# Kernel tuning notes

Hardware: AMD Instinct MI355X
Metric: run time of the kernel (lower is better)

The kernel has to match this reference:

```python
import jax, jax.numpy as jnp
import numpy as np

K = 3  # kernel size along all four dims (kernel_size=3, padding=2=K-1, circular)


def setup_inputs() -> dict:
    key = jax.random.key(0)
    k1, k2, k3 = jax.random.split(key, 3)
    b, c_in, c_out, s = 4, 64, 64, 16
    x = jax.random.normal(k1, (b, c_in, s, s, s, s), dtype=jnp.float32)
    # torch grouped Conv3d weight (out_c*K, c_in, K, K, K) viewed as (K, out_c, c_in, K, K, K):
    # group g (= kernel slice along dim 0) uses weight[g].
    weight = jax.random.normal(k2, (K, c_out, c_in, K, K, K), dtype=jnp.float32) * 0.05
    bias = jax.random.normal(k3, (c_out,), dtype=jnp.float32)
    return {"x": x, "weight": weight, "bias": bias}


def _conv4d_circular(x, weight, bias):
    k = weight.shape[0]
    p = k - 1
    lo, hi = (p + 1) // 2, p // 2  # circular pad split used by do_padding
    b, c = x.shape[0], x.shape[1]
    s0, s1, s2, s3 = x.shape[2:]
    c_out = weight.shape[1]
    # circular-pad the three inner spatial dims only (dim s0 handled via rolls)
    xp = jnp.pad(x, ((0, 0), (0, 0), (0, 0), (lo, hi), (lo, hi), (lo, hi)), mode='wrap')
    # fold s0 into batch: (b*s0, c, S1, S2, S3)
    xr = xp.transpose(0, 2, 1, 3, 4, 5).reshape(b * s0, c, s1 + p, s2 + p, s3 + p)
    # grouped conv with input replicated across groups == k independent VALID 3D convs
    conv = lambda w: jax.lax.conv_general_dilated(
        xr, w, window_strides=(1, 1, 1), padding='VALID',
        dimension_numbers=('NCDHW', 'OIDHW', 'NCDHW'))
    out = jax.vmap(conv)(weight)  # (k, b*s0, c_out, s1, s2, s3)
    out = out.reshape(k, b, s0, c_out, s1, s2, s3).transpose(0, 1, 3, 2, 4, 5, 6)
    # combine kernel slices along dim-0 axis: result[..., t] = sum_i out[i, ..., (t+i) % s0]
    rolled = jnp.stack([jnp.roll(out[i], -i, axis=2) for i in range(k)], axis=0)
    res = rolled.sum(axis=0) + bias[None, :, None, None, None, None]
    shift = (p + 1) // 2  # math.ceil(padding[0] / 2)
    res = jnp.roll(res, shift, axis=2)
    return res  # (b, c_out, s0, s1, s2, s3)


def reference(x, weight, bias):
    return _conv4d_circular(x, weight, bias)
```

## Files before the change

### kernel.cpp

```cpp
#include <hip/hip_runtime.h>

typedef unsigned short u16;
typedef __attribute__((ext_vector_type(8))) __bf16 bf16x8;
typedef __attribute__((ext_vector_type(8))) short short8;
typedef __attribute__((ext_vector_type(4))) short short4v;
typedef __attribute__((ext_vector_type(4))) float floatx4;

__device__ __forceinline__ u16 f2bf(float f){
  unsigned int x = __float_as_uint(f);
  unsigned int r = (x + 0x7fffu + ((x >> 16) & 1u)) >> 16;
  return (u16)r;
}

#define GLL(g, l) __builtin_amdgcn_global_load_lds( \
    (const __attribute__((address_space(1))) void*)(g), \
    (__attribute__((address_space(3))) void*)(l), 16, 0, 0)

__global__ void prep_kernel(const float* __restrict__ x, const float* __restrict__ w,
                            u16* __restrict__ xp, u16* __restrict__ wp){
  __shared__ __attribute__((aligned(16))) u16 I[16384];
  const int bx = blockIdx.x;
  const int tid = threadIdx.x;
  if (bx < 1024){
    const int y = bx & 15, t = (bx >> 4) & 15, b = bx >> 8;
    const int l  = tid & 63;
    const int wv = tid >> 6;
    const float* xb = x + (size_t)b*64*65536 + t*4096 + y*256;

#pragma unroll
    for (int j = 0; j < 16; ++j){
      const int ci = j*4 + wv;
      const float4 f = *(const float4*)(xb + (size_t)ci*65536 + l*4);
      const int o  = ci >> 3;
      const int gp = l ^ o ^ ((o & 1) << 3);
      short4v hv;
      hv[0] = (short)f2bf(f.x);
      hv[1] = (short)f2bf(f.y);
      hv[2] = (short)f2bf(f.z);
      hv[3] = (short)f2bf(f.w);
      *(short4v*)(I + ci*256 + gp*4) = hv;
    }
    __syncthreads();

    const int p  = tid & 7;
    const int r0 = tid >> 3;
    u16* dst = xp + (size_t)bx*16384;
#pragma unroll
    for (int it = 0; it < 8; ++it){
      const int zw = it*32 + r0;
      const int o  = p ^ (zw & 7);
      const int g  = zw >> 2;
      const int gp = g ^ o ^ ((o & 1) << 3);
      const int base = gp*4 + (zw & 3);
      short8 vv;
#pragma unroll
      for (int m = 0; m < 8; ++m)
        vv[m] = (short)I[(o*8 + m)*256 + base];
      *(short8*)(dst + it*2048 + tid*8) = vv;
    }
  } else {
    int idx = (bx - 1024)*256 + tid;
    if (idx < 81*64*64){
      int r  = idx;
      int dw = r % 3; r /= 3;
      int dz = r % 3; r /= 3;
      int dy = r % 3; r /= 3;
      int ci = r & 63; r >>= 6;
      int co = r & 63; r >>= 6;
      int dt = r;
      int tap = ((dt*3 + dy)*3 + dz)*3 + dw;
      int kc = ci >> 5, ci32 = ci & 31;
      wp[tap*4096 + kc*2048 + co*32 + ci32] = f2bf(w[idx]);
    }
  }
}

__global__ __launch_bounds__(256, 2) void conv4d_mfma_v4(
    const u16* __restrict__ xp, const u16* __restrict__ wp,
    const float* __restrict__ bias, float* __restrict__ out)
{
  __shared__ __attribute__((aligned(16))) u16 x_lds[16384];
  __shared__ __attribute__((aligned(16))) u16 a_lds[2][12288];

  const int bx = blockIdx.x;
  const int c = bx & 7, j = bx >> 3;
  const int b = c >> 1, t = j >> 3, y = (c & 1)*8 + (j & 7);

  const int tid  = threadIdx.x;
  const int lane = tid & 63;
  const int wv   = tid >> 6;
  const int wl   = lane & 15;
  const int q    = lane >> 4;

  floatx4 acc[4][4];
#pragma unroll
  for (int zi = 0; zi < 4; ++zi)
#pragma unroll
    for (int mi = 0; mi < 4; ++mi)
      acc[zi][mi] = (floatx4)0.0f;

  auto stage_x = [&](int dtdy){
    const int dt = dtdy / 3, dy = dtdy % 3;
    const int tt = (t + dt + 15) & 15;
    const int yy = (y + dy + 15) & 15;
    const u16* plane = xp + (size_t)(((b*16 + tt)*16) + yy) * 16384;
#pragma unroll
    for (int i = 0; i < 8; ++i)
      GLL(plane + wv*4096 + i*512 + lane*8, x_lds + wv*4096 + i*512);
  };
  auto stage_a = [&](int s, int buf){
    const int dtdy = s / 3, dz = s % 3;
    const int tap0 = ((dtdy/3)*9 + (dtdy%3)*3 + dz)*3;
    const u16* asrc = wp + (size_t)tap0 * 4096;
#pragma unroll
    for (int i = 0; i < 6; ++i)
      GLL(asrc + wv*3072 + i*512 + lane*8, a_lds[buf] + wv*3072 + i*512);
  };

  stage_x(0);
  stage_a(0, 0);
  __syncthreads();

  for (int s = 0; s < 27; ++s){
    const int dz  = s % 3;
    const int cur = s & 1;
    const bool boundary = (dz == 2);
    if (s + 1 < 27 && !boundary)
      stage_a(s + 1, cur ^ 1);

    const u16* ab = a_lds[cur];
#pragma unroll
    for (int dw = 0; dw < 3; ++dw){
      const int ww = (wl + dw + 15) & 15;
      const int wx = ww & 7;
#pragma unroll
      for (int kc = 0; kc < 2; ++kc){
        bf16x8 af[4];
#pragma unroll
        for (int mi = 0; mi < 4; ++mi)
          af[mi] = *(const bf16x8*)(ab + ((dw*2 + kc)*64 + mi*16 + wl)*32 + q*8);
        const int chunk = ((kc*4 + q) ^ wx)*8;
#pragma unroll
        for (int zi = 0; zi < 4; ++zi){
          const int zz = (wv*4 + zi + dz + 15) & 15;
          bf16x8 bf = *(const bf16x8*)(x_lds + (zz*16 + ww)*64 + chunk);
#pragma unroll
          for (int mi = 0; mi < 4; ++mi)
            acc[zi][mi] = __builtin_amdgcn_mfma_f32_16x16x32_bf16(af[mi], bf, acc[zi][mi], 0, 0, 0);
        }
      }
    }

    if (s + 1 >= 27) break;
    if (boundary){
      __syncthreads();
      stage_x(s/3 + 1);
      stage_a(s + 1, cur ^ 1);
      __syncthreads();
    } else {
      __syncthreads();
    }
  }

  float bvals[4][4];
#pragma unroll
  for (int mi = 0; mi < 4; ++mi)
#pragma unroll
    for (int r = 0; r < 4; ++r)
      bvals[mi][r] = bias[mi*16 + q*4 + r];

  float* ob = out + (size_t)b*64*65536 + t*4096 + y*256 + wl;
#pragma unroll
  for (int zi = 0; zi < 4; ++zi){
    const int z = wv*4 + zi;
#pragma unroll
    for (int mi = 0; mi < 4; ++mi){
#pragma unroll
      for (int r = 0; r < 4; ++r){
        const int co = mi*16 + q*4 + r;
        ob[(size_t)co*65536 + z*16] = acc[zi][mi][r] + bvals[mi][r];
      }
    }
  }
}

__global__ void repack_w_kernel(const float* __restrict__ w, u16* __restrict__ wp){
  int idx = blockIdx.x * 256 + threadIdx.x;
  if (idx >= 81*64*64) return;
  int cw  = idx & 31;
  int t1  = idx >> 5;
  int co  = t1 & 63; t1 >>= 6;
  int kc  = t1 & 1;  t1 >>= 1;
  int tap = t1;
  int dw = tap % 3, dz = (tap/3) % 3, dy = (tap/9) % 3, dt = tap/27;
  int ci = kc*32 + cw;
  int in_idx = ((((dt*64 + co)*64 + ci)*3 + dy)*3 + dz)*3 + dw;
  wp[idx] = f2bf(w[in_idx]);
}

__global__ __launch_bounds__(256, 2) void conv4d_mfma_kernel(
    const float* __restrict__ x, const u16* __restrict__ wp,
    const float* __restrict__ bias, float* __restrict__ out)
{
  __shared__ __attribute__((aligned(16))) u16 x_lds[256*72];
  __shared__ __attribute__((aligned(16))) u16 a_lds[3*2*64*32];
  const int bx = blockIdx.x;
  const int y = bx & 15, t = (bx >> 4) & 15, b = bx >> 8;
  const int tid  = threadIdx.x;
  const int lane = tid & 63;
  const int wv   = tid >> 6;
  const int wl   = lane & 15;
  const int q    = lane >> 4;
  floatx4 acc[4][4];
#pragma unroll
  for (int zi = 0; zi < 4; ++zi)
#pragma unroll
    for (int mi = 0; mi < 4; ++mi)
      acc[zi][mi] = (floatx4)0.0f;
  const float* xb = x + (size_t)b * 64 * 65536;
  for (int dt = 0; dt < 3; ++dt){
    const int tt = (t + dt + 15) & 15;
    for (int dy = 0; dy < 3; ++dy){
      const int yy = (y + dy + 15) & 15;
      __syncthreads();
      {
        const float* src = xb + tt*4096 + yy*256 + tid;
#pragma unroll
        for (int oct = 0; oct < 8; ++oct){
          float v[8];
#pragma unroll
          for (int j = 0; j < 8; ++j)
            v[j] = src[(size_t)(oct*8 + j) * 65536];
          short8 vv;
#pragma unroll
          for (int j = 0; j < 8; ++j) vv[j] = (short)f2bf(v[j]);
          *(short8*)(x_lds + tid*72 + oct*8) = vv;
        }
      }
      for (int dz = 0; dz < 3; ++dz){
        const int tap0 = ((dt*3 + dy)*3 + dz)*3;
        __syncthreads();
        {
          const u16* asrc = wp + (size_t)tap0 * 4096;
#pragma unroll
          for (int i = 0; i < 6; ++i){
            int e = (i*256 + tid) * 8;
            *(short8*)(a_lds + e) = *(const short8*)(asrc + e);
          }
        }
        __syncthreads();
#pragma unroll
        for (int dw = 0; dw < 3; ++dw){
          const int ww = (wl + dw + 15) & 15;
#pragma unroll
          for (int kc = 0; kc < 2; ++kc){
            bf16x8 af[4];
#pragma unroll
            for (int mi = 0; mi < 4; ++mi)
              af[mi] = *(const bf16x8*)(a_lds + ((dw*2 + kc)*64 + mi*16 + wl)*32 + q*8);
#pragma unroll
            for (int zi = 0; zi < 4; ++zi){
              const int zz = (wv*4 + zi + dz + 15) & 15;
              bf16x8 bf = *(const bf16x8*)(x_lds + (zz*16 + ww)*72 + kc*32 + q*8);
#pragma unroll
              for (int mi = 0; mi < 4; ++mi)
                acc[zi][mi] = __builtin_amdgcn_mfma_f32_16x16x32_bf16(af[mi], bf, acc[zi][mi], 0, 0, 0);
            }
          }
        }
      }
    }
  }
  float bvals[4][4];
#pragma unroll
  for (int mi = 0; mi < 4; ++mi)
#pragma unroll
    for (int r = 0; r < 4; ++r)
      bvals[mi][r] = bias[mi*16 + q*4 + r];
  float* ob = out + (size_t)b * 64 * 65536 + t*4096 + y*256 + wl;
#pragma unroll
  for (int zi = 0; zi < 4; ++zi){
    const int z = wv*4 + zi;
#pragma unroll
    for (int mi = 0; mi < 4; ++mi){
#pragma unroll
      for (int r = 0; r < 4; ++r){
        const int co = mi*16 + q*4 + r;
        ob[(size_t)co*65536 + z*16] = acc[zi][mi][r] + bvals[mi][r];
      }
    }
  }
}

extern "C" void kernel_launch(void* const* d_in, const int* in_sizes, int n_in,
                              void* d_out, int out_size, void* d_ws, size_t ws_size,
                              hipStream_t stream) {
  const float* x    = (const float*)d_in[0];
  const float* w    = (const float*)d_in[1];
  const float* bias = (const float*)d_in[2];
  float* out = (float*)d_out;

  const size_t xp_bytes = (size_t)1024 * 16384 * 2;
  const size_t wp_bytes = 81*64*64*2;
  if (ws_size >= xp_bytes + wp_bytes){
    u16* xp = (u16*)d_ws;
    u16* wp = (u16*)((char*)d_ws + xp_bytes);
    prep_kernel<<<1024 + 1296, 256, 0, stream>>>(x, w, xp, wp);
    conv4d_mfma_v4<<<1024, 256, 0, stream>>>(xp, wp, bias, out);
  } else {
    u16* wp = (u16*)d_ws;
    repack_w_kernel<<<1296, 256, 0, stream>>>(w, wp);
    conv4d_mfma_kernel<<<1024, 256, 0, stream>>>(x, wp, bias, out);
  }
}
```

Before: 248.8 us.

## Read conv weights directly from global memory, drop weight LDS staging

Weight fragments now load straight from global memory (cached in L1/L2) inside the MFMA loop instead of being double-buffered through LDS. This removes the per-tap weight LDS staging and most __syncthreads, leaving only syncs around each x-plane load. LDS use drops to 32KB, and launch bounds rise to 4 blocks per CU to allow more occupancy. The cost is global-load latency inside the inner loop and possible register pressure from the tighter launch bound.

```diff
diff --git a/kernel.cpp b/kernel.cpp
--- a/kernel.cpp
+++ b/kernel.cpp
@@ -75,12 +75,11 @@
   }
 }
 
-__global__ __launch_bounds__(256, 2) void conv4d_mfma_v4(
+__global__ __launch_bounds__(256, 4) void conv4d_mfma_v5(
     const u16* __restrict__ xp, const u16* __restrict__ wp,
     const float* __restrict__ bias, float* __restrict__ out)
 {
   __shared__ __attribute__((aligned(16))) u16 x_lds[16384];
-  __shared__ __attribute__((aligned(16))) u16 a_lds[2][12288];
 
   const int bx = blockIdx.x;
   const int c = bx & 7, j = bx >> 3;
@@ -99,66 +98,44 @@
     for (int mi = 0; mi < 4; ++mi)
       acc[zi][mi] = (floatx4)0.0f;
 
-  auto stage_x = [&](int dtdy){
+  const u16* wpt = wp + wl*32 + q*8;
+
+  for (int dtdy = 0; dtdy < 9; ++dtdy){
     const int dt = dtdy / 3, dy = dtdy % 3;
     const int tt = (t + dt + 15) & 15;
     const int yy = (y + dy + 15) & 15;
     const u16* plane = xp + (size_t)(((b*16 + tt)*16) + yy) * 16384;
+
+    if (dtdy) __syncthreads();
 #pragma unroll
     for (int i = 0; i < 8; ++i)
       GLL(plane + wv*4096 + i*512 + lane*8, x_lds + wv*4096 + i*512);
-  };
-  auto stage_a = [&](int s, int buf){
-    const int dtdy = s / 3, dz = s % 3;
-    const int tap0 = ((dtdy/3)*9 + (dtdy%3)*3 + dz)*3;
-    const u16* asrc = wp + (size_t)tap0 * 4096;
-#pragma unroll
-    for (int i = 0; i < 6; ++i)
-      GLL(asrc + wv*3072 + i*512 + lane*8, a_lds[buf] + wv*3072 + i*512);
-  };
-
-  stage_x(0);
-  stage_a(0, 0);
-  __syncthreads();
-
-  for (int s = 0; s < 27; ++s){
-    const int dz  = s % 3;
-    const int cur = s & 1;
-    const bool boundary = (dz == 2);
-    if (s + 1 < 27 && !boundary)
-      stage_a(s + 1, cur ^ 1);
-
-    const u16* ab = a_lds[cur];
-#pragma unroll
-    for (int dw = 0; dw < 3; ++dw){
-      const int ww = (wl + dw + 15) & 15;
-      const int wx = ww & 7;
-#pragma unroll
-      for (int kc = 0; kc < 2; ++kc){
-        bf16x8 af[4];
-#pragma unroll
-        for (int mi = 0; mi < 4; ++mi)
-          af[mi] = *(const bf16x8*)(ab + ((dw*2 + kc)*64 + mi*16 + wl)*32 + q*8);
-        const int chunk = ((kc*4 + q) ^ wx)*8;
-#pragma unroll
-        for (int zi = 0; zi < 4; ++zi){
-          const int zz = (wv*4 + zi + dz + 15) & 15;
-          bf16x8 bf = *(const bf16x8*)(x_lds + (zz*16 + ww)*64 + chunk);
+    __syncthreads();
+
+#pragma unroll
+    for (int dz = 0; dz < 3; ++dz){
+      const u16* ab = wpt + (size_t)(dtdy*9 + dz*3) * 4096;
+#pragma unroll
+      for (int dw = 0; dw < 3; ++dw){
+        const int ww = (wl + dw + 15) & 15;
+        const int wx = ww & 7;
+#pragma unroll
+        for (int kc = 0; kc < 2; ++kc){
+          bf16x8 af[4];
 #pragma unroll
           for (int mi = 0; mi < 4; ++mi)
-            acc[zi][mi] = __builtin_amdgcn_mfma_f32_16x16x32_bf16(af[mi], bf, acc[zi][mi], 0, 0, 0);
-        }
-      }
-    }
-
-    if (s + 1 >= 27) break;
-    if (boundary){
-      __syncthreads();
-      stage_x(s/3 + 1);
-      stage_a(s + 1, cur ^ 1);
-      __syncthreads();
-    } else {
-      __syncthreads();
+            af[mi] = *(const bf16x8*)(ab + dw*4096 + kc*2048 + mi*512);
+          const int chunk = ((kc*4 + q) ^ wx)*8;
+#pragma unroll
+          for (int zi = 0; zi < 4; ++zi){
+            const int zz = (wv*4 + zi + dz + 15) & 15;
+            bf16x8 bf = *(const bf16x8*)(x_lds + (zz*16 + ww)*64 + chunk);
+#pragma unroll
+            for (int mi = 0; mi < 4; ++mi)
+              acc[zi][mi] = __builtin_amdgcn_mfma_f32_16x16x32_bf16(af[mi], bf, acc[zi][mi], 0, 0, 0);
+          }
+        }
+      }
     }
   }
 
@@ -306,7 +283,7 @@
     u16* xp = (u16*)d_ws;
     u16* wp = (u16*)((char*)d_ws + xp_bytes);
     prep_kernel<<<1024 + 1296, 256, 0, stream>>>(x, w, xp, wp);
-    conv4d_mfma_v4<<<1024, 256, 0, stream>>>(xp, wp, bias, out);
+    conv4d_mfma_v5<<<1024, 256, 0, stream>>>(xp, wp, bias, out);
   } else {
     u16* wp = (u16*)d_ws;
     repack_w_kernel<<<1296, 256, 0, stream>>>(w, wp);
```

After: 497.5 us. +99.9%, slower.
